# Kernel optimization log

Measured on AMD Instinct MI355X. Metric: run time of the kernel, lower is better.

## Reference

```python
import jax, jax.numpy as jnp
import numpy as np

COST_CLASS = 2.0
COST_SCREW_MID = 5.0
COST_SCREW_HEAD_TIP = 5.0
GAMMA = 2.0
EPS = 1e-8


def _l1_cdist(a, b):
    # a: [N, d], b: [T, d] -> [N, T] pairwise L1 distance
    return jnp.abs(a[:, None, :] - b[None, :, :]).sum(-1)


def _midpoint(s):
    # screw parameterized as (head_xy, tip_xy); midpoint of the segment
    return (s[:, :2] + s[:, 2:]) * 0.5


def setup_inputs() -> dict:
    key = jax.random.key(0)
    k1, k2, k3, k4 = jax.random.split(key, 4)
    bs, nq, nc = 32, 900, 2
    tpi = 30  # targets per image
    total_tgt = bs * tpi
    return {
        "pred_logits": jax.random.normal(k1, (bs, nq, nc), dtype=jnp.float32),
        "pred_screws": jax.random.uniform(k2, (bs, nq, 4), dtype=jnp.float32),
        "tgt_labels": jax.random.randint(k3, (total_tgt,), 0, nc),
        "tgt_screws": jax.random.uniform(k4, (total_tgt, 4), dtype=jnp.float32),
        "num_targets_per_image": tpi,
    }


def reference(pred_logits, pred_screws, tgt_labels, tgt_screws, num_targets_per_image):
    bs, nq, nc = pred_logits.shape
    out_prob = jax.nn.sigmoid(pred_logits.reshape(bs * nq, nc))  # [N, C]
    out_screws = pred_screws.reshape(bs * nq, 4)                 # [N, 4]

    # focal-style classification cost, gathered at target class ids
    neg_cost = out_prob ** GAMMA * -jnp.log1p(-(out_prob - EPS))  # -log(1 - p + eps)
    pos_cost = (1.0 - out_prob) ** GAMMA * -jnp.log(out_prob + EPS)
    cost_class = pos_cost[:, tgt_labels] - neg_cost[:, tgt_labels]  # [N, T]

    # geometric costs: L1 on midpoint, plus L1 on head and tip endpoints
    cost_mid = _l1_cdist(_midpoint(out_screws), _midpoint(tgt_screws))
    cost_head_tip = (_l1_cdist(out_screws[:, :2], tgt_screws[:, :2])
                     + _l1_cdist(out_screws[:, 2:], tgt_screws[:, 2:]))

    C = (COST_SCREW_MID * cost_mid
         + COST_CLASS * cost_class
         + COST_SCREW_HEAD_TIP * cost_head_tip)
    return C.reshape(bs, nq, -1)  # [bs, num_queries, total_targets]
```

## Files before the change

### kernel.cpp

```cpp
#include <hip/hip_runtime.h>
#include <math.h>
#include <stdint.h>


#define BLOCK 256
#define NB 16

typedef float f32x4 __attribute__((ext_vector_type(4)));

__device__ __forceinline__ float class_cost(float l) {
    float p  = 1.0f / (1.0f + expf(-l));
    float om = 1.0f - p;
    float pos = om * om * (-logf(p + 1e-8f));
    float neg = p * p * (-logf(om + 1e-8f));
    return 2.0f * (pos - neg);
}

__global__ __launch_bounds__(BLOCK) void row_desc_kernel(
    const float* __restrict__ logits,
    const float* __restrict__ pscrews,
    float*       __restrict__ ws,
    int N)
{
    int n = blockIdx.x * BLOCK + threadIdx.x;
    if (n >= N) return;
    float4 s = reinterpret_cast<const float4*>(pscrews)[n];
    float2 l = reinterpret_cast<const float2*>(logits)[n];
    f32x4 d0 = {s.x, s.y, s.z, s.w};
    f32x4 d1 = {(s.x + s.z) * 0.5f, (s.y + s.w) * 0.5f, class_cost(l.x), class_cost(l.y)};
    f32x4* w = reinterpret_cast<f32x4*>(ws) + (size_t)n * 2;
    w[0] = d0;
    w[1] = d1;
}

__global__ __launch_bounds__(BLOCK) void matcher_v3(
    const float* __restrict__ ws,
    const int*   __restrict__ tlabels,
    const float* __restrict__ tscrews,
    float*       __restrict__ out,
    int N, int T)
{
    const int tid   = threadIdx.x;
    const int n0    = blockIdx.x * NB;
    const int chunk = tid;
    const bool active = (chunk * 4 + 3) < T;

    float thx[4], thy[4], ttx[4], tty[4], tmx[4], tmy[4];
    int   lab[4];
    if (active) {
        int4 lb = reinterpret_cast<const int4*>(tlabels)[chunk];
        lab[0] = lb.x; lab[1] = lb.y; lab[2] = lb.z; lab[3] = lb.w;
        #pragma unroll
        for (int j = 0; j < 4; ++j) {
            float4 s = reinterpret_cast<const float4*>(tscrews)[chunk * 4 + j];
            thx[j] = s.x; thy[j] = s.y; ttx[j] = s.z; tty[j] = s.w;
            tmx[j] = (s.x + s.z) * 0.5f;
            tmy[j] = (s.y + s.w) * 0.5f;
        }
    }
    if (!active) return;

    const int tq = T >> 2;
    f32x4* outv = reinterpret_cast<f32x4*>(out) + (size_t)n0 * tq + chunk;
    const f32x4* w = reinterpret_cast<const f32x4*>(ws) + (size_t)n0 * 2;

    if (n0 + NB <= N) {
        #pragma unroll
        for (int g = 0; g < NB; g += 4) {
            f32x4 res[4];
            #pragma unroll
            for (int r = 0; r < 4; ++r) {
                f32x4 a = w[(g + r) * 2 + 0];
                f32x4 b = w[(g + r) * 2 + 1];
                float v[4];
                #pragma unroll
                for (int j = 0; j < 4; ++j) {
                    float d = fabsf(a.x - thx[j]) + fabsf(a.y - thy[j])
                            + fabsf(a.z - ttx[j]) + fabsf(a.w - tty[j])
                            + fabsf(b.x - tmx[j]) + fabsf(b.y - tmy[j]);
                    float cc = (lab[j] != 0) ? b.w : b.z;
                    v[j] = fmaf(d, 5.0f, cc);
                }
                res[r].x = v[0]; res[r].y = v[1]; res[r].z = v[2]; res[r].w = v[3];
            }
            #pragma unroll
            for (int r = 0; r < 4; ++r) {
                __builtin_nontemporal_store(res[r], outv + (size_t)(g + r) * tq);
            }
        }
    } else {
        for (int r = 0; r < NB; ++r) {
            const int n = n0 + r;
            if (n >= N) break;
            f32x4 a = w[r * 2 + 0];
            f32x4 b = w[r * 2 + 1];
            f32x4 res;
            #pragma unroll
            for (int j = 0; j < 4; ++j) {
                float d = fabsf(a.x - thx[j]) + fabsf(a.y - thy[j])
                        + fabsf(a.z - ttx[j]) + fabsf(a.w - tty[j])
                        + fabsf(b.x - tmx[j]) + fabsf(b.y - tmy[j]);
                float cc = (lab[j] != 0) ? b.w : b.z;
                res[j] = fmaf(d, 5.0f, cc);
            }
            __builtin_nontemporal_store(res, outv + (size_t)r * tq);
        }
    }
}

__global__ __launch_bounds__(BLOCK) void matcher_fused(
    const float* __restrict__ logits,
    const float* __restrict__ pscrews,
    const int*   __restrict__ tlabels,
    const float* __restrict__ tscrews,
    float*       __restrict__ out,
    int N, int T)
{
    __shared__ float row[NB][8];
    const int tid = threadIdx.x;
    const int n0  = blockIdx.x * NB;

    if (tid < NB && (n0 + tid) < N) {
        const int n = n0 + tid;
        float4 s = reinterpret_cast<const float4*>(pscrews)[n];
        row[tid][0] = s.x; row[tid][1] = s.y;
        row[tid][2] = s.z; row[tid][3] = s.w;
        row[tid][4] = (s.x + s.z) * 0.5f;
        row[tid][5] = (s.y + s.w) * 0.5f;
        row[tid][6] = class_cost(logits[n * 2 + 0]);
        row[tid][7] = class_cost(logits[n * 2 + 1]);
    }

    const int chunk = tid;
    const bool active = (chunk * 4 + 3) < T;
    float thx[4], thy[4], ttx[4], tty[4], tmx[4], tmy[4];
    int   lab[4];
    if (active) {
        int4 lb = reinterpret_cast<const int4*>(tlabels)[chunk];
        lab[0] = lb.x; lab[1] = lb.y; lab[2] = lb.z; lab[3] = lb.w;
        #pragma unroll
        for (int j = 0; j < 4; ++j) {
            float4 s = reinterpret_cast<const float4*>(tscrews)[chunk * 4 + j];
            thx[j] = s.x; thy[j] = s.y; ttx[j] = s.z; tty[j] = s.w;
            tmx[j] = (s.x + s.z) * 0.5f;
            tmy[j] = (s.y + s.w) * 0.5f;
        }
    }
    __syncthreads();
    if (!active) return;

    const int tq = T >> 2;
    for (int r = 0; r < NB; ++r) {
        const int n = n0 + r;
        if (n >= N) break;
        float4 a = *reinterpret_cast<const float4*>(&row[r][0]);
        float4 b = *reinterpret_cast<const float4*>(&row[r][4]);
        f32x4 res;
        #pragma unroll
        for (int j = 0; j < 4; ++j) {
            float d = fabsf(a.x - thx[j]) + fabsf(a.y - thy[j])
                    + fabsf(a.z - ttx[j]) + fabsf(a.w - tty[j])
                    + fabsf(b.x - tmx[j]) + fabsf(b.y - tmy[j]);
            float cc = (lab[j] != 0) ? b.w : b.z;
            res[j] = fmaf(d, 5.0f, cc);
        }
        __builtin_nontemporal_store(res, reinterpret_cast<f32x4*>(out) + (size_t)n * tq + chunk);
    }
}

extern "C" void kernel_launch(void* const* d_in, const int* in_sizes, int n_in,
                              void* d_out, int out_size, void* d_ws, size_t ws_size,
                              hipStream_t stream) {
    const float* logits  = (const float*)d_in[0];
    const float* pscrews = (const float*)d_in[1];
    const int*   tlabels = (const int*)d_in[2];
    const float* tscrews = (const float*)d_in[3];
    float* out = (float*)d_out;

    const int N = in_sizes[1] / 4;
    const int T = in_sizes[2];

    const int blocksB = (N + NB - 1) / NB;

    if (ws_size >= (size_t)N * 8 * sizeof(float)) {
        const int blocksA = (N + BLOCK - 1) / BLOCK;
        row_desc_kernel<<<blocksA, BLOCK, 0, stream>>>(logits, pscrews, (float*)d_ws, N);
        matcher_v3<<<blocksB, BLOCK, 0, stream>>>((const float*)d_ws, tlabels, tscrews,
                                                  out, N, T);
    } else {
        matcher_fused<<<blocksB, BLOCK, 0, stream>>>(logits, pscrews, tlabels, tscrews,
                                                     out, N, T);
    }
}
```

Baseline: 130.1 us.

## Replace row-block matcher with grid-stride flat kernel using LDS-staged targets

The per-row-block matcher is replaced with a grid-stride kernel capped at 2048 blocks, where each thread computes one contiguous float4 of output indexed by flat position. Row and chunk are recovered with a magic-multiply division. Target screws and labels are staged once per block in LDS in a transposed layout. The old kernel left 16 of 256 threads idle (T/4=240) and issued strided stores. The new one keeps every lane busy and writes perfectly contiguous output. In exchange it drops the nontemporal stores, recomputes target midpoints and re-reads LDS per element, and reloads row descriptors from global for each chunk.

```diff
diff --git a/kernel.cpp b/kernel.cpp
--- a/kernel.cpp
+++ b/kernel.cpp
@@ -4,7 +4,7 @@
 
 
 #define BLOCK 256
-#define NB 16
+#define MAXC  256
 
 typedef float f32x4 __attribute__((ext_vector_type(4)));
 
@@ -33,81 +33,54 @@
     w[1] = d1;
 }
 
-__global__ __launch_bounds__(BLOCK) void matcher_v3(
+__global__ __launch_bounds__(BLOCK) void stream_lds_kernel(
     const float* __restrict__ ws,
     const int*   __restrict__ tlabels,
     const float* __restrict__ tscrews,
     float*       __restrict__ out,
-    int N, int T)
+    unsigned total, unsigned TQ, unsigned long long M, int T)
 {
-    const int tid   = threadIdx.x;
-    const int n0    = blockIdx.x * NB;
-    const int chunk = tid;
-    const bool active = (chunk * 4 + 3) < T;
+    __shared__ float4 tA[4][MAXC];
+    __shared__ int4   tL[MAXC];
 
-    float thx[4], thy[4], ttx[4], tty[4], tmx[4], tmy[4];
-    int   lab[4];
-    if (active) {
-        int4 lb = reinterpret_cast<const int4*>(tlabels)[chunk];
-        lab[0] = lb.x; lab[1] = lb.y; lab[2] = lb.z; lab[3] = lb.w;
+    for (int t = threadIdx.x; t < T; t += BLOCK) {
+        float4 s = reinterpret_cast<const float4*>(tscrews)[t];
+        tA[t & 3][t >> 2] = s;
+        reinterpret_cast<int*>(tL)[t] = tlabels[t];
+    }
+    __syncthreads();
+
+    const f32x4* wsv  = reinterpret_cast<const f32x4*>(ws);
+    f32x4*       outv = reinterpret_cast<f32x4*>(out);
+    const unsigned stride = gridDim.x * BLOCK;
+
+    for (unsigned g = blockIdx.x * BLOCK + threadIdx.x; g < total; g += stride) {
+        unsigned row   = (unsigned)(((unsigned long long)g * M) >> 38);
+        unsigned chunk = g - row * TQ;
+
+        f32x4 a = wsv[row * 2 + 0];
+        f32x4 b = wsv[row * 2 + 1];
+        int4 lb = tL[chunk];
+        int labs[4] = {lb.x, lb.y, lb.z, lb.w};
+
+        float v[4];
         #pragma unroll
         for (int j = 0; j < 4; ++j) {
-            float4 s = reinterpret_cast<const float4*>(tscrews)[chunk * 4 + j];
-            thx[j] = s.x; thy[j] = s.y; ttx[j] = s.z; tty[j] = s.w;
-            tmx[j] = (s.x + s.z) * 0.5f;
-            tmy[j] = (s.y + s.w) * 0.5f;
+            float4 s = tA[j][chunk];
+            float tmx = (s.x + s.z) * 0.5f;
+            float tmy = (s.y + s.w) * 0.5f;
+            float d = fabsf(a.x - s.x) + fabsf(a.y - s.y)
+                    + fabsf(a.z - s.z) + fabsf(a.w - s.w)
+                    + fabsf(b.x - tmx) + fabsf(b.y - tmy);
+            float cc = (labs[j] != 0) ? b.w : b.z;
+            v[j] = fmaf(d, 5.0f, cc);
         }
-    }
-    if (!active) return;
-
-    const int tq = T >> 2;
-    f32x4* outv = reinterpret_cast<f32x4*>(out) + (size_t)n0 * tq + chunk;
-    const f32x4* w = reinterpret_cast<const f32x4*>(ws) + (size_t)n0 * 2;
-
-    if (n0 + NB <= N) {
-        #pragma unroll
-        for (int g = 0; g < NB; g += 4) {
-            f32x4 res[4];
-            #pragma unroll
-            for (int r = 0; r < 4; ++r) {
-                f32x4 a = w[(g + r) * 2 + 0];
-                f32x4 b = w[(g + r) * 2 + 1];
-                float v[4];
-                #pragma unroll
-                for (int j = 0; j < 4; ++j) {
-                    float d = fabsf(a.x - thx[j]) + fabsf(a.y - thy[j])
-                            + fabsf(a.z - ttx[j]) + fabsf(a.w - tty[j])
-                            + fabsf(b.x - tmx[j]) + fabsf(b.y - tmy[j]);
-                    float cc = (lab[j] != 0) ? b.w : b.z;
-                    v[j] = fmaf(d, 5.0f, cc);
-                }
-                res[r].x = v[0]; res[r].y = v[1]; res[r].z = v[2]; res[r].w = v[3];
-            }
-            #pragma unroll
-            for (int r = 0; r < 4; ++r) {
-                __builtin_nontemporal_store(res[r], outv + (size_t)(g + r) * tq);
-            }
-        }
-    } else {
-        for (int r = 0; r < NB; ++r) {
-            const int n = n0 + r;
-            if (n >= N) break;
-            f32x4 a = w[r * 2 + 0];
-            f32x4 b = w[r * 2 + 1];
-            f32x4 res;
-            #pragma unroll
-            for (int j = 0; j < 4; ++j) {
-                float d = fabsf(a.x - thx[j]) + fabsf(a.y - thy[j])
-                        + fabsf(a.z - ttx[j]) + fabsf(a.w - tty[j])
-                        + fabsf(b.x - tmx[j]) + fabsf(b.y - tmy[j]);
-                float cc = (lab[j] != 0) ? b.w : b.z;
-                res[j] = fmaf(d, 5.0f, cc);
-            }
-            __builtin_nontemporal_store(res, outv + (size_t)r * tq);
-        }
+        f32x4 res = {v[0], v[1], v[2], v[3]};
+        outv[g] = res;
     }
 }
 
+#define NB 16
 __global__ __launch_bounds__(BLOCK) void matcher_fused(
     const float* __restrict__ logits,
     const float* __restrict__ pscrews,
@@ -180,15 +153,24 @@
     const int N = in_sizes[1] / 4;
     const int T = in_sizes[2];
 
-    const int blocksB = (N + NB - 1) / NB;
+    const bool ws_ok = ws_size >= (size_t)N * 8 * sizeof(float);
+    const bool fits  = (T % 4 == 0) && (T / 4 <= MAXC);
 
-    if (ws_size >= (size_t)N * 8 * sizeof(float)) {
+    if (ws_ok && fits) {
+        const unsigned TQ    = (unsigned)(T / 4);
+        const unsigned total = (unsigned)N * TQ;
+        const unsigned long long M = ((1ULL << 38) + TQ - 1) / TQ;
+
         const int blocksA = (N + BLOCK - 1) / BLOCK;
         row_desc_kernel<<<blocksA, BLOCK, 0, stream>>>(logits, pscrews, (float*)d_ws, N);
-        matcher_v3<<<blocksB, BLOCK, 0, stream>>>((const float*)d_ws, tlabels, tscrews,
-                                                  out, N, T);
+
+        unsigned need = (total + BLOCK - 1) / BLOCK;
+        const int blocksB = (int)(need < 2048u ? need : 2048u);
+        stream_lds_kernel<<<blocksB, BLOCK, 0, stream>>>((const float*)d_ws, tlabels,
+                                                         tscrews, out, total, TQ, M, T);
     } else {
-        matcher_fused<<<blocksB, BLOCK, 0, stream>>>(logits, pscrews, tlabels, tscrews,
-                                                     out, N, T);
+        const int blocks = (N + NB - 1) / NB;
+        matcher_fused<<<blocks, BLOCK, 0, stream>>>(logits, pscrews, tlabels, tscrews,
+                                                    out, N, T);
     }
 }
```

Measured after the change: 129.1 us. No clear change (-0.8%).
